# Performance work log

Hardware: AMD Instinct MI355X
Metric: run time of the kernel (lower is better)

The kernel has to match this reference:

```python
import jax, jax.numpy as jnp
import numpy as np

EMB = 1024
NH = 16
HS = EMB // NH  # 64


def setup_inputs() -> dict:
    key = jax.random.key(0)
    k_x, k_wqkv, k_bqkv, k_wo, k_bo = jax.random.split(key, 5)
    x = jax.random.normal(k_x, (4, 2048, EMB), dtype=jnp.float32)
    s = 1.0 / np.sqrt(EMB)
    # torch nn.Linear weight is [out, in]; store as [in, out] for x @ W
    w_qkv = jax.random.uniform(k_wqkv, (EMB, 3 * EMB), dtype=jnp.float32, minval=-s, maxval=s)
    b_qkv = jax.random.uniform(k_bqkv, (3 * EMB,), dtype=jnp.float32, minval=-s, maxval=s)
    w_out = jax.random.uniform(k_wo, (EMB, EMB), dtype=jnp.float32, minval=-s, maxval=s)
    b_out = jax.random.uniform(k_bo, (EMB,), dtype=jnp.float32, minval=-s, maxval=s)
    return {"x": x, "w_qkv": w_qkv, "b_qkv": b_qkv, "w_out": w_out, "b_out": b_out}


def reference(x, w_qkv, b_qkv, w_out, b_out):
    B, T, C = x.shape
    qkv = x @ w_qkv + b_qkv  # [B, T, 3*C]
    q, k, v = jnp.split(qkv, 3, axis=-1)
    # [B, T, C] -> [B, nh, T, hs]
    def heads(t):
        return t.reshape(B, T, NH, HS).transpose(0, 2, 1, 3)
    q, k, v = heads(q), heads(k), heads(v)
    scores = jnp.einsum('bhqd,bhkd->bhqk', q, k) / jnp.sqrt(jnp.float32(HS))
    attn = jax.nn.softmax(scores, axis=-1)  # dropout=0 -> identity
    out = jnp.einsum('bhqk,bhkd->bhqd', attn, v)
    out = out.transpose(0, 2, 1, 3).reshape(B, T, NH * HS)
    return out @ w_out + b_out
```

## Files before the change

### kernel.cpp

```cpp
#include <hip/hip_runtime.h>

typedef unsigned short u16;
typedef unsigned int u32;
typedef __attribute__((ext_vector_type(8))) __bf16 bf16x8;
typedef __attribute__((ext_vector_type(4))) __bf16 bf16x4;
typedef __attribute__((ext_vector_type(4))) float f32x4;

#define GLD_AS1 const __attribute__((address_space(1))) void*
#define GLD_AS3 __attribute__((address_space(3))) void*

__device__ __forceinline__ u16 f2b(float f) {
  u32 u = __builtin_bit_cast(u32, f);
  u += 0x7fffu + ((u >> 16) & 1u);
  return (u16)(u >> 16);
}

__global__ void cvt_x_kernel(const float* __restrict__ in, u16* __restrict__ out, int n) {
  int i4 = (blockIdx.x * blockDim.x + threadIdx.x) * 4;
  if (i4 < n) {
    float4 v = *(const float4*)(in + i4);
    ushort4 o;
    o.x = f2b(v.x); o.y = f2b(v.y); o.z = f2b(v.z); o.w = f2b(v.w);
    *(ushort4*)(out + i4) = o;
  }
}

__global__ void transpose_w_kernel(const float* __restrict__ src, u16* __restrict__ dst,
                                   int R, int C) {
  __shared__ float tile[32][33];
  int c0 = blockIdx.x * 32, r0 = blockIdx.y * 32;
  int tx = threadIdx.x & 31, ty = threadIdx.x >> 5;
  #pragma unroll
  for (int i = ty; i < 32; i += 8)
    tile[i][tx] = src[(size_t)(r0 + i) * C + c0 + tx];
  __syncthreads();
  #pragma unroll
  for (int i = ty; i < 32; i += 8)
    dst[(size_t)(c0 + i) * R + r0 + tx] = f2b(tile[tx][i]);
}

__global__ void transpose_v_kernel(const u16* __restrict__ v, u16* __restrict__ vt) {
  __shared__ u16 tile[64][68];
  int t0 = blockIdx.x * 64;
  int bh = blockIdx.y;
  int tx = threadIdx.x & 31, ty = threadIdx.x >> 5;
  const u16* src = v + (size_t)bh * 2048 * 64;
  u16* dst = vt + (size_t)bh * 64 * 2048;
  #pragma unroll
  for (int i = ty; i < 64; i += 8)
    *(u32*)&tile[i][tx * 2] = *(const u32*)&src[(size_t)(t0 + i) * 64 + tx * 2];
  __syncthreads();
  #pragma unroll
  for (int d = ty; d < 64; d += 8) {
    u32 a = tile[tx * 2][d];
    u32 b = tile[tx * 2 + 1][d];
    *(u32*)&dst[(size_t)d * 2048 + t0 + tx * 2] = a | (b << 16);
  }
}

template <int MODE>
__global__ __launch_bounds__(256)
void gemm_kernel(const u16* __restrict__ A, const u16* __restrict__ Bt,
                 const float* __restrict__ bias,
                 u16* __restrict__ qo, u16* __restrict__ ko, u16* __restrict__ vo,
                 float* __restrict__ outF, int N, int K) {
  __shared__ u16 As[128 * 64];
  __shared__ u16 Bs[128 * 64];
  const int tid = threadIdx.x;
  const int lane = tid & 63, wave = tid >> 6;
  const int m0 = blockIdx.x * 128, n0 = blockIdx.y * 128;
  const int wm = (wave >> 1) * 64, wn = (wave & 1) * 64;
  const int lr = lane & 15, lg = lane >> 4;

  const int rA = tid >> 3;
  const int kbs = ((tid & 7) * 16) ^ ((rA & 7) << 4);

  const char* Ab = (const char*)(A + (size_t)m0 * K);
  const char* Bb = (const char*)(Bt + (size_t)n0 * K);
  const size_t strideB = (size_t)K * 2;

  f32x4 acc[4][4] = {};
  const int swr = (lr & 7) << 4;

  const int nk = K >> 6;
  for (int kt = 0; kt < nk; ++kt) {
    const int kb0 = kt * 128;
    #pragma unroll
    for (int i = 0; i < 4; ++i)
      __builtin_amdgcn_global_load_lds(
          (GLD_AS1)(Ab + (size_t)(i * 32 + rA) * strideB + kb0 + kbs),
          (GLD_AS3)((char*)As + i * 4096 + tid * 16), 16, 0, 0);
    #pragma unroll
    for (int i = 0; i < 4; ++i)
      __builtin_amdgcn_global_load_lds(
          (GLD_AS1)(Bb + (size_t)(i * 32 + rA) * strideB + kb0 + kbs),
          (GLD_AS3)((char*)Bs + i * 4096 + tid * 16), 16, 0, 0);
    __syncthreads();

    bf16x8 af[4][2], bfr[4][2];
    #pragma unroll
    for (int m = 0; m < 4; ++m) {
      int row = wm + m * 16 + lr;
      #pragma unroll
      for (int s = 0; s < 2; ++s)
        af[m][s] = *(const bf16x8*)((const char*)As + row * 128 + ((s * 64 + lg * 16) ^ swr));
    }
    #pragma unroll
    for (int n = 0; n < 4; ++n) {
      int row = wn + n * 16 + lr;
      #pragma unroll
      for (int s = 0; s < 2; ++s)
        bfr[n][s] = *(const bf16x8*)((const char*)Bs + row * 128 + ((s * 64 + lg * 16) ^ swr));
    }
    #pragma unroll
    for (int m = 0; m < 4; ++m)
      #pragma unroll
      for (int n = 0; n < 4; ++n) {
        acc[m][n] = __builtin_amdgcn_mfma_f32_16x16x32_bf16(af[m][0], bfr[n][0], acc[m][n], 0, 0, 0);
        acc[m][n] = __builtin_amdgcn_mfma_f32_16x16x32_bf16(af[m][1], bfr[n][1], acc[m][n], 0, 0, 0);
      }
    __syncthreads();
  }

  #pragma unroll
  for (int n = 0; n < 4; ++n) {
    const int col = n0 + wn + n * 16 + lr;
    const float bv = bias[col];
    #pragma unroll
    for (int m = 0; m < 4; ++m) {
      const int rowb = m0 + wm + m * 16 + lg * 4;
      #pragma unroll
      for (int j = 0; j < 4; ++j) {
        float val = acc[m][n][j] + bv;
        int row = rowb + j;
        if (MODE == 0) {
          int which = col >> 10, c = col & 1023;
          int h = c >> 6, d = c & 63;
          int b = row >> 11, t = row & 2047;
          if (which == 0) val *= 0.18033688011112042f;
          u16* dst = which == 0 ? qo : (which == 1 ? ko : vo);
          dst[((size_t)(b * 16 + h) * 2048 + t) * 64 + d] = f2b(val);
        } else {
          outF[(size_t)row * N + col] = val;
        }
      }
    }
  }
}

__global__ __launch_bounds__(256)
void attn_kernel(const u16* __restrict__ Q, const u16* __restrict__ Kg,
                 const u16* __restrict__ Vt, u16* __restrict__ att) {
  const int tid = threadIdx.x;
  const int wave = tid >> 6, lane = tid & 63;
  const int lr = lane & 15, lg = lane >> 4;
  const int bh = blockIdx.x;
  const int q0 = blockIdx.y * 128;
  const int b = bh >> 4, h = bh & 15;

  const u16* Qh = Q + (size_t)bh * 2048 * 64;
  const char* Khb = (const char*)(Kg + (size_t)bh * 2048 * 64);
  const char* Vhb = (const char*)(Vt + (size_t)bh * 64 * 2048);

  __shared__ u16 Ks[3][64 * 64];
  __shared__ u16 Vs[3][64 * 64];

  const int rS = tid >> 3;
  const int cS = ((tid & 7) * 16) ^ ((rS & 7) << 4);

  bf16x8 qf[2][2];
  #pragma unroll
  for (int m = 0; m < 2; ++m)
    #pragma unroll
    for (int s = 0; s < 2; ++s)
      qf[m][s] = *(const bf16x8*)(Qh + (size_t)(q0 + wave * 32 + m * 16 + lr) * 64 + s * 32 + lg * 8);

  f32x4 acc[2][4] = {};
  f32x4 rlv[2] = {};

#define STAGE(T, BUF)                                                          \
  {                                                                            \
    _Pragma("unroll")                                                          \
    for (int i = 0; i < 2; ++i)                                                \
      __builtin_amdgcn_global_load_lds(                                        \
          (GLD_AS1)(Khb + (size_t)((T) * 64 + i * 32 + rS) * 128 + cS),        \
          (GLD_AS3)((char*)Ks[BUF] + i * 4096 + tid * 16), 16, 0, 0);          \
    _Pragma("unroll")                                                          \
    for (int i = 0; i < 2; ++i)                                                \
      __builtin_amdgcn_global_load_lds(                                        \
          (GLD_AS1)(Vhb + (size_t)(i * 32 + rS) * 4096 + (T) * 128 + cS),      \
          (GLD_AS3)((char*)Vs[BUF] + i * 4096 + tid * 16), 16, 0, 0);          \
  }

  STAGE(0, 0);
  STAGE(1, 1);

  for (int kt = 0; kt < 32; ++kt) {
    if (kt == 31) { asm volatile("s_waitcnt vmcnt(0)" ::: "memory"); }
    else          { asm volatile("s_waitcnt vmcnt(4)" ::: "memory"); }
    __builtin_amdgcn_sched_barrier(0);
    __builtin_amdgcn_s_barrier();
    if (kt < 30) STAGE(kt + 2, (kt + 2) % 3);
    const int cur = kt % 3;

    f32x4 sf[2][4] = {};
    __builtin_amdgcn_s_setprio(1);
    #pragma unroll
    for (int n = 0; n < 4; ++n) {
      const int rk = n * 16 + lr;
      #pragma unroll
      for (int s = 0; s < 2; ++s) {
        bf16x8 kf = *(const bf16x8*)((const char*)Ks[cur] + rk * 128 +
                                     ((s * 64 + lg * 16) ^ ((lr & 7) << 4)));
        sf[0][n] = __builtin_amdgcn_mfma_f32_16x16x32_bf16(kf, qf[0][s], sf[0][n], 0, 0, 0);
        sf[1][n] = __builtin_amdgcn_mfma_f32_16x16x32_bf16(kf, qf[1][s], sf[1][n], 0, 0, 0);
      }
    }
    __builtin_amdgcn_s_setprio(0);

    bf16x8 pa[2][2];
    #pragma unroll
    for (int m = 0; m < 2; ++m)
      #pragma unroll
      for (int ks = 0; ks < 2; ++ks) {
        f32x4 p0, p1;
        #pragma unroll
        for (int j = 0; j < 4; ++j) p0[j] = __builtin_amdgcn_exp2f(sf[m][2 * ks][j]);
        #pragma unroll
        for (int j = 0; j < 4; ++j) p1[j] = __builtin_amdgcn_exp2f(sf[m][2 * ks + 1][j]);
        rlv[m] += p0;
        rlv[m] += p1;
        #pragma unroll
        for (int j = 0; j < 4; ++j) { pa[m][ks][j] = (__bf16)p0[j]; pa[m][ks][4 + j] = (__bf16)p1[j]; }
      }

    __builtin_amdgcn_s_setprio(1);
    #pragma unroll
    for (int ks = 0; ks < 2; ++ks) {
      #pragma unroll
      for (int d = 0; d < 4; ++d) {
        const int rv = d * 16 + lr;
        bf16x4 v0 = *(const bf16x4*)((const char*)Vs[cur] + rv * 128 +
                                     ((64 * ks + 8 * lg) ^ ((lr & 7) << 4)));
        bf16x4 v1 = *(const bf16x4*)((const char*)Vs[cur] + rv * 128 +
                                     ((64 * ks + 8 * lg + 32) ^ ((lr & 7) << 4)));
        bf16x8 vf;
        #pragma unroll
        for (int e = 0; e < 4; ++e) { vf[e] = v0[e]; vf[4 + e] = v1[e]; }
        acc[0][d] = __builtin_amdgcn_mfma_f32_16x16x32_bf16(vf, pa[0][ks], acc[0][d], 0, 0, 0);
        acc[1][d] = __builtin_amdgcn_mfma_f32_16x16x32_bf16(vf, pa[1][ks], acc[1][d], 0, 0, 0);
      }
    }
    __builtin_amdgcn_s_setprio(0);
  }

  #pragma unroll
  for (int m = 0; m < 2; ++m) {
    float rl = rlv[m][0] + rlv[m][1] + rlv[m][2] + rlv[m][3];
    rl += __shfl_xor(rl, 16);
    rl += __shfl_xor(rl, 32);
    const float inv = 1.0f / rl;
    const int t = q0 + wave * 32 + m * 16 + lr;
    #pragma unroll
    for (int d = 0; d < 4; ++d) {
      bf16x4 ov;
      #pragma unroll
      for (int j = 0; j < 4; ++j) ov[j] = (__bf16)(acc[m][d][j] * inv);
      *(bf16x4*)&att[((size_t)b * 2048 + t) * 1024 + h * 64 + d * 16 + lg * 4] = ov;
    }
  }
#undef STAGE
}

extern "C" void kernel_launch(void* const* d_in, const int* in_sizes, int n_in,
                              void* d_out, int out_size, void* d_ws, size_t ws_size,
                              hipStream_t stream) {
  const float* x     = (const float*)d_in[0];
  const float* w_qkv = (const float*)d_in[1];
  const float* b_qkv = (const float*)d_in[2];
  const float* w_out = (const float*)d_in[3];
  const float* b_out = (const float*)d_in[4];
  float* out = (float*)d_out;

  char* ws = (char*)d_ws;
  const size_t MB = 1024 * 1024;
  u16* xb    = (u16*)(ws);
  u16* wqkvt = (u16*)(ws + 16 * MB);
  u16* woutt = (u16*)(ws + 22 * MB);
  u16* qb    = (u16*)(ws + 24 * MB);
  u16* kb    = (u16*)(ws + 40 * MB);
  u16* vb    = (u16*)(ws + 56 * MB);
  u16* vtb   = (u16*)(ws + 72 * MB);
  u16* attb  = xb;

  {
    int n = 4 * 2048 * 1024;
    cvt_x_kernel<<<(n / 4 + 255) / 256, 256, 0, stream>>>(x, xb, n);
  }
  transpose_w_kernel<<<dim3(3072 / 32, 1024 / 32), 256, 0, stream>>>(w_qkv, wqkvt, 1024, 3072);
  transpose_w_kernel<<<dim3(1024 / 32, 1024 / 32), 256, 0, stream>>>(w_out, woutt, 1024, 1024);

  gemm_kernel<0><<<dim3(8192 / 128, 3072 / 128), 256, 0, stream>>>(
      xb, wqkvt, b_qkv, qb, kb, vb, nullptr, 3072, 1024);

  transpose_v_kernel<<<dim3(2048 / 64, 64), 256, 0, stream>>>(vb, vtb);

  attn_kernel<<<dim3(64, 16), 256, 0, stream>>>(qb, kb, vtb, attb);

  gemm_kernel<1><<<dim3(8192 / 128, 1024 / 128), 256, 0, stream>>>(
      attb, woutt, b_out, nullptr, nullptr, nullptr, out, 1024, 1024);
}
```

Baseline: 213.9 us.

## Permute V transpose layout for single 16-byte LDS reads and MFMA row sums

Permutes the key-position order inside each 64-wide chunk of the transposed V buffer so the attention kernel can fetch each V fragment with one 16-byte LDS read instead of two 8-byte reads plus repacking. The score and PV loops are restructured per 32-key half so the exponentials feed straight into the PV MFMAs. The softmax denominator is now computed with an extra MFMA against a vector of ones instead of VALU adds and cross-lane shuffles. This adds two MFMAs per half-tile and sums the bf16-rounded probabilities, which changes rounding slightly.

```diff
diff --git a/kernel.cpp b/kernel.cpp
--- a/kernel.cpp
+++ b/kernel.cpp
@@ -50,11 +50,14 @@
   for (int i = ty; i < 64; i += 8)
     *(u32*)&tile[i][tx * 2] = *(const u32*)&src[(size_t)(t0 + i) * 64 + tx * 2];
   __syncthreads();
+  const int c = tx * 2;
+  const int e = c & 3, g = (c >> 2) & 3, hi = (c >> 4) & 1;
+  const int cp = (c & 32) | (8 * g + 4 * hi + e);
   #pragma unroll
   for (int d = ty; d < 64; d += 8) {
-    u32 a = tile[tx * 2][d];
-    u32 b = tile[tx * 2 + 1][d];
-    *(u32*)&dst[(size_t)d * 2048 + t0 + tx * 2] = a | (b << 16);
+    u32 a = tile[c][d];
+    u32 b = tile[c + 1][d];
+    *(u32*)&dst[(size_t)d * 2048 + t0 + cp] = a | (b << 16);
   }
 }
 
@@ -175,8 +178,12 @@
     for (int s = 0; s < 2; ++s)
       qf[m][s] = *(const bf16x8*)(Qh + (size_t)(q0 + wave * 32 + m * 16 + lr) * 64 + s * 32 + lg * 8);
 
+  bf16x8 ones;
+  #pragma unroll
+  for (int e = 0; e < 8; ++e) ones[e] = (__bf16)1.0f;
+
   f32x4 acc[2][4] = {};
-  f32x4 rlv[2] = {};
+  f32x4 accl[2] = {};
 
 #define STAGE(T, BUF)                                                          \
   {                                                                            \
@@ -203,63 +210,50 @@
     if (kt < 30) STAGE(kt + 2, (kt + 2) % 3);
     const int cur = kt % 3;
 
-    f32x4 sf[2][4] = {};
-    __builtin_amdgcn_s_setprio(1);
-    #pragma unroll
-    for (int n = 0; n < 4; ++n) {
-      const int rk = n * 16 + lr;
+    #pragma unroll
+    for (int ks = 0; ks < 2; ++ks) {
+      f32x4 sf0[2] = {}, sf1[2] = {};
+      __builtin_amdgcn_s_setprio(1);
       #pragma unroll
       for (int s = 0; s < 2; ++s) {
-        bf16x8 kf = *(const bf16x8*)((const char*)Ks[cur] + rk * 128 +
-                                     ((s * 64 + lg * 16) ^ ((lr & 7) << 4)));
-        sf[0][n] = __builtin_amdgcn_mfma_f32_16x16x32_bf16(kf, qf[0][s], sf[0][n], 0, 0, 0);
-        sf[1][n] = __builtin_amdgcn_mfma_f32_16x16x32_bf16(kf, qf[1][s], sf[1][n], 0, 0, 0);
+        bf16x8 kf0 = *(const bf16x8*)((const char*)Ks[cur] + (2 * ks * 16 + lr) * 128 +
+                                      ((s * 64 + lg * 16) ^ ((lr & 7) << 4)));
+        sf0[0] = __builtin_amdgcn_mfma_f32_16x16x32_bf16(kf0, qf[0][s], sf0[0], 0, 0, 0);
+        sf0[1] = __builtin_amdgcn_mfma_f32_16x16x32_bf16(kf0, qf[1][s], sf0[1], 0, 0, 0);
+        bf16x8 kf1 = *(const bf16x8*)((const char*)Ks[cur] + ((2 * ks + 1) * 16 + lr) * 128 +
+                                      ((s * 64 + lg * 16) ^ ((lr & 7) << 4)));
+        sf1[0] = __builtin_amdgcn_mfma_f32_16x16x32_bf16(kf1, qf[0][s], sf1[0], 0, 0, 0);
+        sf1[1] = __builtin_amdgcn_mfma_f32_16x16x32_bf16(kf1, qf[1][s], sf1[1], 0, 0, 0);
       }
-    }
-    __builtin_amdgcn_s_setprio(0);
-
-    bf16x8 pa[2][2];
-    #pragma unroll
-    for (int m = 0; m < 2; ++m)
-      #pragma unroll
-      for (int ks = 0; ks < 2; ++ks) {
-        f32x4 p0, p1;
+      __builtin_amdgcn_s_setprio(0);
+
+      bf16x8 pa[2];
+      #pragma unroll
+      for (int m = 0; m < 2; ++m)
         #pragma unroll
-        for (int j = 0; j < 4; ++j) p0[j] = __builtin_amdgcn_exp2f(sf[m][2 * ks][j]);
-        #pragma unroll
-        for (int j = 0; j < 4; ++j) p1[j] = __builtin_amdgcn_exp2f(sf[m][2 * ks + 1][j]);
-        rlv[m] += p0;
-        rlv[m] += p1;
-        #pragma unroll
-        for (int j = 0; j < 4; ++j) { pa[m][ks][j] = (__bf16)p0[j]; pa[m][ks][4 + j] = (__bf16)p1[j]; }
-      }
-
-    __builtin_amdgcn_s_setprio(1);
-    #pragma unroll
-    for (int ks = 0; ks < 2; ++ks) {
+        for (int j = 0; j < 4; ++j) {
+          pa[m][j]     = (__bf16)__builtin_amdgcn_exp2f(sf0[m][j]);
+          pa[m][4 + j] = (__bf16)__builtin_amdgcn_exp2f(sf1[m][j]);
+        }
+
+      __builtin_amdgcn_s_setprio(1);
+      accl[0] = __builtin_amdgcn_mfma_f32_16x16x32_bf16(ones, pa[0], accl[0], 0, 0, 0);
+      accl[1] = __builtin_amdgcn_mfma_f32_16x16x32_bf16(ones, pa[1], accl[1], 0, 0, 0);
       #pragma unroll
       for (int d = 0; d < 4; ++d) {
         const int rv = d * 16 + lr;
-        bf16x4 v0 = *(const bf16x4*)((const char*)Vs[cur] + rv * 128 +
-                                     ((64 * ks + 8 * lg) ^ ((lr & 7) << 4)));
-        bf16x4 v1 = *(const bf16x4*)((const char*)Vs[cur] + rv * 128 +
-                                     ((64 * ks + 8 * lg + 32) ^ ((lr & 7) << 4)));
-        bf16x8 vf;
-        #pragma unroll
-        for (int e = 0; e < 4; ++e) { vf[e] = v0[e]; vf[4 + e] = v1[e]; }
-        acc[0][d] = __builtin_amdgcn_mfma_f32_16x16x32_bf16(vf, pa[0][ks], acc[0][d], 0, 0, 0);
-        acc[1][d] = __builtin_amdgcn_mfma_f32_16x16x32_bf16(vf, pa[1][ks], acc[1][d], 0, 0, 0);
+        bf16x8 vf = *(const bf16x8*)((const char*)Vs[cur] + rv * 128 +
+                                     ((64 * ks + 16 * lg) ^ ((lr & 7) << 4)));
+        acc[0][d] = __builtin_amdgcn_mfma_f32_16x16x32_bf16(vf, pa[0], acc[0][d], 0, 0, 0);
+        acc[1][d] = __builtin_amdgcn_mfma_f32_16x16x32_bf16(vf, pa[1], acc[1][d], 0, 0, 0);
       }
-    }
-    __builtin_amdgcn_s_setprio(0);
+      __builtin_amdgcn_s_setprio(0);
+    }
   }
 
   #pragma unroll
   for (int m = 0; m < 2; ++m) {
-    float rl = rlv[m][0] + rlv[m][1] + rlv[m][2] + rlv[m][3];
-    rl += __shfl_xor(rl, 16);
-    rl += __shfl_xor(rl, 32);
-    const float inv = 1.0f / rl;
+    const float inv = 1.0f / accl[m][0];
     const int t = q0 + wave * 32 + m * 16 + lr;
     #pragma unroll
     for (int d = 0; d < 4; ++d) {
```

Measured after the change: 208.7 us. -2.4%, faster.
